# Optimization experiments

Hardware: AMD Instinct MI355X
Metric: run time of the kernel (lower is better)

## Reference

```python
import jax, jax.numpy as jnp
import numpy as np

# Instant-NGP multi-resolution hash grid encoder hyperparameters
L = 16                 # n_levels
F = 2                  # n_features_per_level
LOG2_T = 19
T = 1 << LOG2_T        # hash table size per level
BASE_RES = 16
FINEST_RES = 512
DATA_RANGE = 1.0
N_POINTS = 1 << 20

_scale = np.exp((np.log(FINEST_RES) - np.log(BASE_RES)) / (L - 1))
RES = np.floor(BASE_RES * _scale ** np.arange(L)).astype(np.int32)  # [L]
PRIMES = jnp.asarray(np.array([1, 2654435761, 805459861], dtype=np.uint32))
# 8 corner offsets of the unit cube, bit d of corner i -> offset along dim d
_corners_np = np.array([[(i >> d) & 1 for d in range(3)] for i in range(8)])
CORNERS_U = jnp.asarray(_corners_np.astype(np.uint32))   # [8,3] for coords
CORNERS_B = jnp.asarray(_corners_np.astype(bool))        # [8,3] for weights


def hashgrid_encode(x, table):
    """x: [N,3] in [0, DATA_RANGE]; table: [L, T, F]. Returns [N, L*F]."""
    xn = x / DATA_RANGE  # normalize to [0,1]
    outs = []
    for l in range(L):  # fixed small loop over levels
        s = xn * jnp.float32(RES[l])        # [N,3] scaled coords
        pos = jnp.floor(s)
        frac = s - pos                      # [N,3] in [0,1)
        pos_u = pos.astype(jnp.uint32)
        corner = pos_u[:, None, :] + CORNERS_U[None]        # [N,8,3]
        h = corner * PRIMES                                  # uint32 wraps
        idx = (h[..., 0] ^ h[..., 1] ^ h[..., 2]) & jnp.uint32(T - 1)  # [N,8]
        feats = table[l][idx]                                # gather [N,8,F]
        # trilinear interpolation weights per corner
        w = jnp.where(CORNERS_B[None], frac[:, None, :], 1.0 - frac[:, None, :]).prod(-1)  # [N,8]
        outs.append(jnp.einsum('nc,ncf->nf', w, feats))      # [N,F]
    return jnp.concatenate(outs, axis=-1)                    # [N, L*F]


def setup_inputs() -> dict:
    key = jax.random.key(0)
    k1, k2 = jax.random.split(key)
    x = jax.random.uniform(k1, (N_POINTS, 3), dtype=jnp.float32) * DATA_RANGE
    # NGP init: small uniform-ish values; scale randn by 1e-4
    table = jax.random.normal(k2, (L, T, F), dtype=jnp.float32) * 1e-4
    return {"x": x, "table": table}


def reference(x, table):
    return hashgrid_encode(x, table)
```

## Files before the change

kernel.cpp:

```cpp
#include <hip/hip_runtime.h>
#include <math.h>


#define LEVELS 16
#define LOG2_T 19
#define TMASK ((1u << LOG2_T) - 1u)

typedef float f32x2 __attribute__((ext_vector_type(2)));
typedef float f32x4 __attribute__((ext_vector_type(4)));

struct ResArgs { float r[LEVELS]; };

__device__ __forceinline__ f32x2 encode_one(
    const f32x2* __restrict__ tbl, float rf,
    float x0, float x1, float x2)
{
    const float sx = x0 * rf, sy = x1 * rf, sz = x2 * rf;
    const float px = floorf(sx), py = floorf(sy), pz = floorf(sz);
    const float fx = sx - px, fy = sy - py, fz = sz - pz;
    const unsigned ix = (unsigned)px, iy = (unsigned)py, iz = (unsigned)pz;

    const unsigned hx0 = ix;
    const unsigned hx1 = ix + 1u;
    const unsigned hy0 = iy * 2654435761u;
    const unsigned hy1 = hy0 + 2654435761u;
    const unsigned hz0 = iz * 805459861u;
    const unsigned hz1 = hz0 + 805459861u;

    const unsigned i000 = (hx0 ^ hy0 ^ hz0) & TMASK;
    const unsigned i100 = (hx1 ^ hy0 ^ hz0) & TMASK;
    const unsigned i010 = (hx0 ^ hy1 ^ hz0) & TMASK;
    const unsigned i110 = (hx1 ^ hy1 ^ hz0) & TMASK;
    const unsigned i001 = (hx0 ^ hy0 ^ hz1) & TMASK;
    const unsigned i101 = (hx1 ^ hy0 ^ hz1) & TMASK;
    const unsigned i011 = (hx0 ^ hy1 ^ hz1) & TMASK;
    const unsigned i111 = (hx1 ^ hy1 ^ hz1) & TMASK;

    const f32x2 c000 = tbl[i000];
    const f32x2 c100 = tbl[i100];
    const f32x2 c010 = tbl[i010];
    const f32x2 c110 = tbl[i110];
    const f32x2 c001 = tbl[i001];
    const f32x2 c101 = tbl[i101];
    const f32x2 c011 = tbl[i011];
    const f32x2 c111 = tbl[i111];

    const float wx1 = fx, wx0 = 1.0f - fx;
    const float wy1 = fy, wy0 = 1.0f - fy;
    const float wz1 = fz, wz0 = 1.0f - fz;
    const float w00 = wy0 * wz0;
    const float w10 = wy1 * wz0;
    const float w01 = wy0 * wz1;
    const float w11 = wy1 * wz1;

    float w, a0, a1;
    w = wx0 * w00; a0 = w * c000.x;          a1 = w * c000.y;
    w = wx1 * w00; a0 = fmaf(w, c100.x, a0); a1 = fmaf(w, c100.y, a1);
    w = wx0 * w10; a0 = fmaf(w, c010.x, a0); a1 = fmaf(w, c010.y, a1);
    w = wx1 * w10; a0 = fmaf(w, c110.x, a0); a1 = fmaf(w, c110.y, a1);
    w = wx0 * w01; a0 = fmaf(w, c001.x, a0); a1 = fmaf(w, c001.y, a1);
    w = wx1 * w01; a0 = fmaf(w, c101.x, a0); a1 = fmaf(w, c101.y, a1);
    w = wx0 * w11; a0 = fmaf(w, c011.x, a0); a1 = fmaf(w, c011.y, a1);
    w = wx1 * w11; a0 = fmaf(w, c111.x, a0); a1 = fmaf(w, c111.y, a1);

    f32x2 o; o.x = a0; o.y = a1;
    return o;
}

__global__ __launch_bounds__(256) void ngp_gather_level(
    const float* __restrict__ x,
    const float* __restrict__ table,
    f32x2* __restrict__ out_t,
    float rf, int level, unsigned n)
{
    const unsigned p = blockIdx.x * 256u + threadIdx.x;
    if (p >= n) return;
    const float x0 = __builtin_nontemporal_load(&x[3u*p]);
    const float x1 = __builtin_nontemporal_load(&x[3u*p+1u]);
    const float x2 = __builtin_nontemporal_load(&x[3u*p+2u]);
    const f32x2* __restrict__ tbl =
        (const f32x2*)table + ((size_t)level << LOG2_T);
    f32x2 o = encode_one(tbl, rf, x0, x1, x2);
    __builtin_nontemporal_store(o, &out_t[(size_t)level * n + p]);
}

__global__ __launch_bounds__(256) void ngp_transpose_lds(
    const f32x2* __restrict__ out_t,
    f32x4* __restrict__ out,
    unsigned n)
{
    __shared__ f32x2 lds[256][LEVELS + 1];
    const unsigned t = threadIdx.x;
    const unsigned p0 = blockIdx.x * 256u;

    #pragma unroll
    for (int l = 0; l < LEVELS; ++l)
        lds[t][l] = out_t[(size_t)l * n + p0 + t];
    __syncthreads();

    #pragma unroll
    for (int j = 0; j < 8; ++j) {
        const unsigned g = (unsigned)j * 256u + t;
        const unsigned p = g >> 3, q = g & 7u;
        const f32x2 a = lds[p][2u*q];
        const f32x2 b = lds[p][2u*q + 1u];
        f32x4 v; v.x = a.x; v.y = a.y; v.z = b.x; v.w = b.y;
        __builtin_nontemporal_store(v, &out[(size_t)p0 * 8u + g]);
    }
}

__global__ __launch_bounds__(256) void ngp_encode_direct(
    const float* __restrict__ x,
    const float* __restrict__ table,
    f32x2* __restrict__ out,
    ResArgs res,
    unsigned n_points)
{
    const unsigned t = blockIdx.x * 256u + threadIdx.x;
    const unsigned level = t & (LEVELS - 1u);
    const unsigned p = t >> 4;
    if (p >= n_points) return;
    const float x0 = x[3u*p], x1 = x[3u*p+1u], x2 = x[3u*p+2u];
    const f32x2* __restrict__ tbl =
        (const f32x2*)table + ((size_t)level << LOG2_T);
    f32x2 o = encode_one(tbl, res.r[level], x0, x1, x2);
    __builtin_nontemporal_store(o, &out[t]);
}

extern "C" void kernel_launch(void* const* d_in, const int* in_sizes, int n_in,
                              void* d_out, int out_size, void* d_ws, size_t ws_size,
                              hipStream_t stream) {
    const float* x     = (const float*)d_in[0];
    const float* table = (const float*)d_in[1];
    const unsigned n_points = (unsigned)(in_sizes[0] / 3);

    ResArgs res;
    const double scale = exp((log(512.0) - log(16.0)) / 15.0);
    for (int l = 0; l < LEVELS; ++l) {
        res.r[l] = (float)floor(16.0 * pow(scale, (double)l));
    }

    const size_t scratch_needed = (size_t)LEVELS * n_points * sizeof(f32x2);
    const bool fits = (ws_size >= scratch_needed) && (n_points % 256u == 0u);

    if (fits) {
        f32x2* out_t = (f32x2*)d_ws;
        const unsigned nblk = n_points / 256u;
        for (int l = 0; l < LEVELS; ++l) {
            ngp_gather_level<<<dim3(nblk), dim3(256), 0, stream>>>(
                x, table, out_t, res.r[l], l, n_points);
        }
        ngp_transpose_lds<<<dim3(nblk), dim3(256), 0, stream>>>(
            out_t, (f32x4*)d_out, n_points);
    } else {
        const unsigned total = n_points * LEVELS;
        const unsigned nblk = (total + 255u) / 256u;
        ngp_encode_direct<<<dim3(nblk), dim3(256), 0, stream>>>(
            x, table, (f32x2*)d_out, res, n_points);
    }
}
```

Baseline: 638.2 us.

## Process two points per thread in level gather and halve transpose LDS tile

Each gather thread now loads two points' coordinates as three vectorized float2 loads and writes both results with one float4 store, so the gather launch uses half as many threads. Each thread keeps 16 independent table gathers in flight, which exposes more memory-level parallelism per wave. The transpose kernel now stages its block in two halves of 128 points with coalesced per-level reads, which halves LDS use per block. This trades fewer waves in flight and extra barriers for wider memory accesses.

```diff
diff --git a/kernel.cpp b/kernel.cpp
--- a/kernel.cpp
+++ b/kernel.cpp
@@ -67,21 +67,29 @@
     return o;
 }
 
-__global__ __launch_bounds__(256) void ngp_gather_level(
+__global__ __launch_bounds__(256) void ngp_gather_level2(
     const float* __restrict__ x,
     const float* __restrict__ table,
     f32x2* __restrict__ out_t,
     float rf, int level, unsigned n)
 {
-    const unsigned p = blockIdx.x * 256u + threadIdx.x;
-    if (p >= n) return;
-    const float x0 = __builtin_nontemporal_load(&x[3u*p]);
-    const float x1 = __builtin_nontemporal_load(&x[3u*p+1u]);
-    const float x2 = __builtin_nontemporal_load(&x[3u*p+2u]);
+    const unsigned gid = blockIdx.x * 256u + threadIdx.x;
+    const unsigned p0 = 2u * gid;
+    if (p0 >= n) return;
+
+    const f32x2* __restrict__ xv = (const f32x2*)x;
+    const f32x2 u0 = __builtin_nontemporal_load(&xv[3u*gid]);
+    const f32x2 u1 = __builtin_nontemporal_load(&xv[3u*gid+1u]);
+    const f32x2 u2 = __builtin_nontemporal_load(&xv[3u*gid+2u]);
+
     const f32x2* __restrict__ tbl =
         (const f32x2*)table + ((size_t)level << LOG2_T);
-    f32x2 o = encode_one(tbl, rf, x0, x1, x2);
-    __builtin_nontemporal_store(o, &out_t[(size_t)level * n + p]);
+
+    const f32x2 oa = encode_one(tbl, rf, u0.x, u0.y, u1.x);
+    const f32x2 ob = encode_one(tbl, rf, u1.y, u2.x, u2.y);
+
+    f32x4 v; v.x = oa.x; v.y = oa.y; v.z = ob.x; v.w = ob.y;
+    __builtin_nontemporal_store(v, (f32x4*)&out_t[(size_t)level * n + p0]);
 }
 
 __global__ __launch_bounds__(256) void ngp_transpose_lds(
@@ -89,23 +97,31 @@
     f32x4* __restrict__ out,
     unsigned n)
 {
-    __shared__ f32x2 lds[256][LEVELS + 1];
+    __shared__ f32x2 lds[128][LEVELS + 1];
     const unsigned t = threadIdx.x;
-    const unsigned p0 = blockIdx.x * 256u;
+    const unsigned pbase = blockIdx.x * 256u;
 
     #pragma unroll
-    for (int l = 0; l < LEVELS; ++l)
-        lds[t][l] = out_t[(size_t)l * n + p0 + t];
-    __syncthreads();
-
-    #pragma unroll
-    for (int j = 0; j < 8; ++j) {
-        const unsigned g = (unsigned)j * 256u + t;
-        const unsigned p = g >> 3, q = g & 7u;
-        const f32x2 a = lds[p][2u*q];
-        const f32x2 b = lds[p][2u*q + 1u];
-        f32x4 v; v.x = a.x; v.y = a.y; v.z = b.x; v.w = b.y;
-        __builtin_nontemporal_store(v, &out[(size_t)p0 * 8u + g]);
+    for (int half = 0; half < 2; ++half) {
+        const unsigned p0 = pbase + (unsigned)half * 128u;
+        #pragma unroll
+        for (int j = 0; j < 8; ++j) {
+            const unsigned idx = (unsigned)j * 256u + t;
+            const unsigned l  = idx >> 7;
+            const unsigned pp = idx & 127u;
+            lds[pp][l] = out_t[(size_t)l * n + p0 + pp];
+        }
+        __syncthreads();
+        #pragma unroll
+        for (int j = 0; j < 4; ++j) {
+            const unsigned g = (unsigned)j * 256u + t;
+            const unsigned p = g >> 3, q = g & 7u;
+            const f32x2 a = lds[p][2u*q];
+            const f32x2 b = lds[p][2u*q + 1u];
+            f32x4 v; v.x = a.x; v.y = a.y; v.z = b.x; v.w = b.y;
+            __builtin_nontemporal_store(v, &out[(size_t)p0 * 8u + g]);
+        }
+        __syncthreads();
     }
 }
 
@@ -141,16 +157,17 @@
     }
 
     const size_t scratch_needed = (size_t)LEVELS * n_points * sizeof(f32x2);
-    const bool fits = (ws_size >= scratch_needed) && (n_points % 256u == 0u);
+    const bool fits = (ws_size >= scratch_needed) && (n_points % 512u == 0u);
 
     if (fits) {
         f32x2* out_t = (f32x2*)d_ws;
-        const unsigned nblk = n_points / 256u;
+        const unsigned gblk = n_points / 512u;
         for (int l = 0; l < LEVELS; ++l) {
-            ngp_gather_level<<<dim3(nblk), dim3(256), 0, stream>>>(
+            ngp_gather_level2<<<dim3(gblk), dim3(256), 0, stream>>>(
                 x, table, out_t, res.r[l], l, n_points);
         }
-        ngp_transpose_lds<<<dim3(nblk), dim3(256), 0, stream>>>(
+        const unsigned tblk = n_points / 256u;
+        ngp_transpose_lds<<<dim3(tblk), dim3(256), 0, stream>>>(
             out_t, (f32x4*)d_out, n_points);
     } else {
         const unsigned total = n_points * LEVELS;
```

After: 678.1 us. +6.3%, slower.

## Replace per-level gather launches with persistent atomic work-queue kernel

Applied to the files above, without the earlier changes.

Swaps the sixteen per-level gather launches for one persistent kernel of 2048 blocks that pulls (level, 256-point tile) work items from a global atomic counter in level-major order. This removes per-launch gaps and lets blocks flow across level boundaries while still keeping each level's hash table hot in cache. The transpose kernel now stages 128 points at a time in a smaller LDS tile with coalesced per-level loads. In exchange it adds a memset, an atomic and two block barriers per tile, and depends on the workspace having room for the counter.

```diff
diff --git a/kernel.cpp b/kernel.cpp
--- a/kernel.cpp
+++ b/kernel.cpp
@@ -5,6 +5,8 @@
 #define LEVELS 16
 #define LOG2_T 19
 #define TMASK ((1u << LOG2_T) - 1u)
+#define QBLOCKS 2048u
+#define TILE_PTS 256u
 
 typedef float f32x2 __attribute__((ext_vector_type(2)));
 typedef float f32x4 __attribute__((ext_vector_type(4)));
@@ -19,40 +21,22 @@
     const float px = floorf(sx), py = floorf(sy), pz = floorf(sz);
     const float fx = sx - px, fy = sy - py, fz = sz - pz;
     const unsigned ix = (unsigned)px, iy = (unsigned)py, iz = (unsigned)pz;
-
-    const unsigned hx0 = ix;
-    const unsigned hx1 = ix + 1u;
-    const unsigned hy0 = iy * 2654435761u;
-    const unsigned hy1 = hy0 + 2654435761u;
-    const unsigned hz0 = iz * 805459861u;
-    const unsigned hz1 = hz0 + 805459861u;
-
-    const unsigned i000 = (hx0 ^ hy0 ^ hz0) & TMASK;
-    const unsigned i100 = (hx1 ^ hy0 ^ hz0) & TMASK;
-    const unsigned i010 = (hx0 ^ hy1 ^ hz0) & TMASK;
-    const unsigned i110 = (hx1 ^ hy1 ^ hz0) & TMASK;
-    const unsigned i001 = (hx0 ^ hy0 ^ hz1) & TMASK;
-    const unsigned i101 = (hx1 ^ hy0 ^ hz1) & TMASK;
-    const unsigned i011 = (hx0 ^ hy1 ^ hz1) & TMASK;
-    const unsigned i111 = (hx1 ^ hy1 ^ hz1) & TMASK;
-
-    const f32x2 c000 = tbl[i000];
-    const f32x2 c100 = tbl[i100];
-    const f32x2 c010 = tbl[i010];
-    const f32x2 c110 = tbl[i110];
-    const f32x2 c001 = tbl[i001];
-    const f32x2 c101 = tbl[i101];
-    const f32x2 c011 = tbl[i011];
-    const f32x2 c111 = tbl[i111];
-
+    const unsigned hx0 = ix, hx1 = ix + 1u;
+    const unsigned hy0 = iy * 2654435761u, hy1 = hy0 + 2654435761u;
+    const unsigned hz0 = iz * 805459861u,  hz1 = hz0 + 805459861u;
+    const f32x2 c000 = tbl[(hx0 ^ hy0 ^ hz0) & TMASK];
+    const f32x2 c100 = tbl[(hx1 ^ hy0 ^ hz0) & TMASK];
+    const f32x2 c010 = tbl[(hx0 ^ hy1 ^ hz0) & TMASK];
+    const f32x2 c110 = tbl[(hx1 ^ hy1 ^ hz0) & TMASK];
+    const f32x2 c001 = tbl[(hx0 ^ hy0 ^ hz1) & TMASK];
+    const f32x2 c101 = tbl[(hx1 ^ hy0 ^ hz1) & TMASK];
+    const f32x2 c011 = tbl[(hx0 ^ hy1 ^ hz1) & TMASK];
+    const f32x2 c111 = tbl[(hx1 ^ hy1 ^ hz1) & TMASK];
     const float wx1 = fx, wx0 = 1.0f - fx;
     const float wy1 = fy, wy0 = 1.0f - fy;
     const float wz1 = fz, wz0 = 1.0f - fz;
-    const float w00 = wy0 * wz0;
-    const float w10 = wy1 * wz0;
-    const float w01 = wy0 * wz1;
-    const float w11 = wy1 * wz1;
-
+    const float w00 = wy0 * wz0, w10 = wy1 * wz0;
+    const float w01 = wy0 * wz1, w11 = wy1 * wz1;
     float w, a0, a1;
     w = wx0 * w00; a0 = w * c000.x;          a1 = w * c000.y;
     w = wx1 * w00; a0 = fmaf(w, c100.x, a0); a1 = fmaf(w, c100.y, a1);
@@ -62,9 +46,75 @@
     w = wx1 * w01; a0 = fmaf(w, c101.x, a0); a1 = fmaf(w, c101.y, a1);
     w = wx0 * w11; a0 = fmaf(w, c011.x, a0); a1 = fmaf(w, c011.y, a1);
     w = wx1 * w11; a0 = fmaf(w, c111.x, a0); a1 = fmaf(w, c111.y, a1);
-
     f32x2 o; o.x = a0; o.y = a1;
     return o;
+}
+
+__global__ __launch_bounds__(256, 8) void ngp_gather_queue(
+    const float* __restrict__ x,
+    const float* __restrict__ table,
+    f32x2* __restrict__ out_t,
+    unsigned* __restrict__ counter,
+    ResArgs res,
+    unsigned n)
+{
+    const unsigned tpl = n / TILE_PTS;
+    const unsigned total = tpl * LEVELS;
+    __shared__ unsigned s_tile;
+
+    for (;;) {
+        if (threadIdx.x == 0u) s_tile = atomicAdd(counter, 1u);
+        __syncthreads();
+        const unsigned t = s_tile;
+        __syncthreads();
+        if (t >= total) break;
+
+        const unsigned level = t / tpl;
+        const unsigned base  = (t - level * tpl) * TILE_PTS;
+        const unsigned p = base + threadIdx.x;
+
+        const float x0 = __builtin_nontemporal_load(&x[3u*p]);
+        const float x1 = __builtin_nontemporal_load(&x[3u*p+1u]);
+        const float x2 = __builtin_nontemporal_load(&x[3u*p+2u]);
+
+        const f32x2* __restrict__ tbl =
+            (const f32x2*)table + ((size_t)level << LOG2_T);
+        f32x2 o = encode_one(tbl, res.r[level], x0, x1, x2);
+        __builtin_nontemporal_store(o, &out_t[(size_t)level * n + p]);
+    }
+}
+
+__global__ __launch_bounds__(256) void ngp_transpose_lds(
+    const f32x2* __restrict__ out_t,
+    f32x4* __restrict__ out,
+    unsigned n)
+{
+    __shared__ f32x2 lds[128][LEVELS + 1];
+    const unsigned t = threadIdx.x;
+    const unsigned pbase = blockIdx.x * 256u;
+
+    #pragma unroll
+    for (int half = 0; half < 2; ++half) {
+        const unsigned p0 = pbase + (unsigned)half * 128u;
+        #pragma unroll
+        for (int j = 0; j < 8; ++j) {
+            const unsigned idx = (unsigned)j * 256u + t;
+            const unsigned l  = idx >> 7;
+            const unsigned pp = idx & 127u;
+            lds[pp][l] = out_t[(size_t)l * n + p0 + pp];
+        }
+        __syncthreads();
+        #pragma unroll
+        for (int j = 0; j < 4; ++j) {
+            const unsigned g = (unsigned)j * 256u + t;
+            const unsigned p = g >> 3, q = g & 7u;
+            const f32x2 a = lds[p][2u*q];
+            const f32x2 b = lds[p][2u*q + 1u];
+            f32x4 v; v.x = a.x; v.y = a.y; v.z = b.x; v.w = b.y;
+            __builtin_nontemporal_store(v, &out[(size_t)p0 * 8u + g]);
+        }
+        __syncthreads();
+    }
 }
 
 __global__ __launch_bounds__(256) void ngp_gather_level(
@@ -82,31 +132,6 @@
         (const f32x2*)table + ((size_t)level << LOG2_T);
     f32x2 o = encode_one(tbl, rf, x0, x1, x2);
     __builtin_nontemporal_store(o, &out_t[(size_t)level * n + p]);
-}
-
-__global__ __launch_bounds__(256) void ngp_transpose_lds(
-    const f32x2* __restrict__ out_t,
-    f32x4* __restrict__ out,
-    unsigned n)
-{
-    __shared__ f32x2 lds[256][LEVELS + 1];
-    const unsigned t = threadIdx.x;
-    const unsigned p0 = blockIdx.x * 256u;
-
-    #pragma unroll
-    for (int l = 0; l < LEVELS; ++l)
-        lds[t][l] = out_t[(size_t)l * n + p0 + t];
-    __syncthreads();
-
-    #pragma unroll
-    for (int j = 0; j < 8; ++j) {
-        const unsigned g = (unsigned)j * 256u + t;
-        const unsigned p = g >> 3, q = g & 7u;
-        const f32x2 a = lds[p][2u*q];
-        const f32x2 b = lds[p][2u*q + 1u];
-        f32x4 v; v.x = a.x; v.y = a.y; v.z = b.x; v.w = b.y;
-        __builtin_nontemporal_store(v, &out[(size_t)p0 * 8u + g]);
-    }
 }
 
 __global__ __launch_bounds__(256) void ngp_encode_direct(
@@ -141,9 +166,20 @@
     }
 
     const size_t scratch_needed = (size_t)LEVELS * n_points * sizeof(f32x2);
-    const bool fits = (ws_size >= scratch_needed) && (n_points % 256u == 0u);
+    const bool scratch_ok = (ws_size >= scratch_needed) &&
+                            (n_points % 256u == 0u);
+    const bool queue_ok = scratch_ok &&
+                          (ws_size >= scratch_needed + sizeof(unsigned));
 
-    if (fits) {
+    if (queue_ok) {
+        f32x2* out_t = (f32x2*)d_ws;
+        unsigned* counter = (unsigned*)((char*)d_ws + scratch_needed);
+        hipMemsetAsync(counter, 0, sizeof(unsigned), stream);
+        ngp_gather_queue<<<dim3(QBLOCKS), dim3(256), 0, stream>>>(
+            x, table, out_t, counter, res, n_points);
+        ngp_transpose_lds<<<dim3(n_points / 256u), dim3(256), 0, stream>>>(
+            out_t, (f32x4*)d_out, n_points);
+    } else if (scratch_ok) {
         f32x2* out_t = (f32x2*)d_ws;
         const unsigned nblk = n_points / 256u;
         for (int l = 0; l < LEVELS; ++l) {
```

Result: slower. 1.036 ms (+62.3%).
